# Performance work log

Measured on AMD Instinct MI355X. Metric: run time of the kernel, lower is better.

## Reference

```python
import jax, jax.numpy as jnp
import numpy as np

N_USERS = 50000
N_ITEMS = 100000
N_ENT = 200000
N_REL_TOTAL = 32  # n_relations * 2
DIM = 64
N_INTENTS = 2
N_LAYERS = 1
B = 4096
E_KG = 2_000_000
E_UI_HALF = 1_000_000  # user->item interactions; symmetrized to 2M directed edges


def setup_inputs() -> dict:
    key = jax.random.key(0)
    ks = jax.random.split(key, 16)
    s = 0.05  # xavier-ish scale
    user_emb = jax.random.normal(ks[0], (N_USERS, DIM), jnp.float32) * s
    entity_emb = jax.random.normal(ks[1], (N_ENT, DIM), jnp.float32) * s
    relation_emb = jax.random.normal(ks[2], (N_REL_TOTAL, DIM), jnp.float32) * s
    intent_weights = jax.random.normal(ks[3], (N_INTENTS, N_REL_TOTAL), jnp.float32) * s
    router_w = jax.random.normal(ks[4], (N_INTENTS, DIM), jnp.float32) * s
    router_b = jnp.zeros((N_INTENTS,), jnp.float32)
    kg_w = jax.random.normal(ks[5], (N_LAYERS, DIM, DIM), jnp.float32) * (1.0 / np.sqrt(DIM))
    item2entity = jax.random.randint(ks[6], (N_ITEMS,), 0, N_ENT)
    kg_src = jax.random.randint(ks[7], (E_KG,), 0, N_ENT)
    kg_dst = jax.random.randint(ks[8], (E_KG,), 0, N_ENT)
    kg_rel = jax.random.randint(ks[9], (E_KG,), 0, N_REL_TOTAL)
    # UI bipartite graph, symmetrically normalized (D^-1/2 A D^-1/2), as in _build_ui_graph
    rng = np.random.default_rng(0)
    uu = rng.integers(0, N_USERS, E_UI_HALF)
    ii = rng.integers(0, N_ITEMS, E_UI_HALF) + N_USERS
    rows = np.concatenate([uu, ii])
    cols = np.concatenate([ii, uu])
    n_nodes = N_USERS + N_ITEMS
    deg = np.bincount(rows, minlength=n_nodes).astype(np.float32)
    dinv = np.where(deg > 0, deg ** -0.5, 0.0).astype(np.float32)
    ui_vals = jnp.asarray(dinv[rows] * dinv[cols])
    ui_row = jnp.asarray(rows.astype(np.int32))
    ui_col = jnpseq = jnp.asarray(cols.astype(np.int32))
    u = jax.random.randint(ks[10], (B,), 0, N_USERS)
    i = jax.random.randint(ks[11], (B,), 0, N_ITEMS)
    neg_i = jax.random.randint(ks[12], (B,), 0, N_ITEMS)
    return dict(u=u, i=i, neg_i=neg_i,
                user_emb=user_emb, entity_emb=entity_emb, relation_emb=relation_emb,
                intent_weights=intent_weights, router_w=router_w, router_b=router_b,
                kg_w=kg_w, ui_vals=ui_vals,
                item2entity=item2entity, kg_src=kg_src, kg_dst=kg_dst, kg_rel=kg_rel,
                ui_row=ui_row, ui_col=ui_col)


def _l2norm(x):
    return x / jnp.maximum(jnp.linalg.norm(x, axis=-1, keepdims=True), 1e-12)


def reference(u, i, neg_i, user_emb, entity_emb, relation_emb, intent_weights,
              router_w, router_b, kg_w, ui_vals, item2entity, kg_src, kg_dst,
              kg_rel, ui_row, ui_col):
    n_ent = entity_emb.shape[0]
    # ---- _propagate_kg (dropout in eval mode = identity) ----
    x = entity_emb
    gate = jax.nn.sigmoid(relation_emb[kg_rel])  # [E, D]
    deg = jax.ops.segment_sum(jnp.ones(kg_dst.shape[0], jnp.float32), kg_dst,
                              num_segments=n_ent)
    deg = jnp.maximum(deg, 1.0)[:, None]
    for l in range(kg_w.shape[0]):
        msg = (x[kg_src] @ kg_w[l].T) * gate           # gather + linear + gate
        agg = jax.ops.segment_sum(msg, kg_dst, num_segments=n_ent)
        x = _l2norm(jax.nn.elu(agg / deg + x))
    item_kg = x[item2entity]                            # [n_items, D]
    # ---- _propagate_ui: sparse normalized adj propagation ----
    all_emb = jnp.concatenate([user_emb, item_kg], 0)
    n_nodes = all_emb.shape[0]
    embs = [all_emb]
    for _ in range(N_LAYERS):
        all_emb = jax.ops.segment_sum(ui_vals[:, None] * all_emb[ui_col], ui_row,
                                      num_segments=n_nodes)
        embs.append(all_emb)
    final = jnp.mean(jnp.stack(embs, 1), 1)
    n_users = user_emb.shape[0]
    u_prop, i_prop = final[:n_users], final[n_users:]
    # ---- intent mixing ----
    intent_dist = jax.nn.softmax(u_prop @ router_w.T + router_b, axis=-1)
    intent_emb = jax.nn.softmax(intent_weights, axis=-1) @ relation_emb
    ue = u_prop + intent_dist @ intent_emb
    ie = i_prop + item_kg
    pos = jnp.sum(ue[u] * ie[i], 1)
    neg = jnp.sum(ue[u] * ie[neg_i], 1)
    return pos, neg
```

## Files before the change

### kernel.cpp

```cpp
#include <hip/hip_runtime.h>
#include <math.h>

#define N_USERS 50000
#define N_ITEMS 100000
#define N_ENT   200000
#define N_NODES (N_USERS + N_ITEMS)
#define N_REL   32
#define DIM     64

#define NB_KG  391
#define NB_UI  586
#define NB_TOT (NB_KG + NB_UI)
#define CAPD   4096
#define NSCAT  768

__device__ __forceinline__ unsigned short f2bf(float f) {
    unsigned u = __float_as_uint(f);
    u += 0x7FFFu + ((u >> 16) & 1u);
    return (unsigned short)(u >> 16);
}
__device__ __forceinline__ float bf_lo(unsigned v) { return __uint_as_float(v << 16); }
__device__ __forceinline__ float bf_hi(unsigned v) { return __uint_as_float(v & 0xFFFF0000u); }
__device__ __forceinline__ int getbit(const unsigned* m, int i) {
    return (m[i >> 5] >> (i & 31)) & 1;
}

__global__ __launch_bounds__(512) void mm_scatter(const float* __restrict__ x,
                                                  const float* __restrict__ w,
                                                  unsigned short* __restrict__ y16,
                                                  int n_ent,
                                                  const int* __restrict__ kg_src,
                                                  const int* __restrict__ kg_dst,
                                                  const int* __restrict__ kg_rel,
                                                  const int* __restrict__ ui_row,
                                                  const int* __restrict__ ui_col,
                                                  const float* __restrict__ ui_vals,
                                                  const unsigned* __restrict__ ent_mask,
                                                  const unsigned* __restrict__ node_mask,
                                                  int* __restrict__ bcur,
                                                  unsigned int* __restrict__ kgrec,
                                                  int* __restrict__ uirec,
                                                  float* __restrict__ uval,
                                                  int e_kg, int e_ui) {
    __shared__ __align__(16) char smem[49152];
    int tid = threadIdx.x;

    if (blockIdx.x < NSCAT) {
        int* h     = (int*)smem;
        int* lbase = h + NB_TOT;
        int n = e_kg + e_ui;
        int nchunks = (n + 4095) >> 12;
        for (int c = blockIdx.x; c < nchunks; c += NSCAT) {
            int base = c << 12;
            for (int i = tid; i < NB_TOT; i += 512) h[i] = 0;
            __syncthreads();
            unsigned int rec[8];
            float val[8];
            int bk[8];
            #pragma unroll
            for (int j = 0; j < 8; j++) {
                int e = base + j * 512 + tid;
                bk[j] = -1;
                if (e < n) {
                    if (e < e_kg) {
                        int d = kg_dst[e];
                        if (getbit(ent_mask, d)) {
                            bk[j]  = d >> 9;
                            rec[j] = (unsigned int)kg_src[e]
                                     | ((unsigned int)kg_rel[e] << 18)
                                     | ((unsigned int)(d & 511) << 23);
                            atomicAdd(&h[bk[j]], 1);
                        }
                    } else {
                        int i2 = e - e_kg;
                        int r  = ui_row[i2];
                        if (getbit(node_mask, r)) {
                            bk[j]  = NB_KG + (r >> 8);
                            rec[j] = (unsigned int)ui_col[i2]
                                     | ((unsigned int)(r & 255) << 18);
                            val[j] = ui_vals[i2];
                            atomicAdd(&h[bk[j]], 1);
                        }
                    }
                }
            }
            __syncthreads();
            for (int i = tid; i < NB_TOT; i += 512) {
                int cc = h[i];
                lbase[i] = cc ? atomicAdd(&bcur[i], cc) : 0;
            }
            __syncthreads();
            #pragma unroll
            for (int j = 0; j < 8; j++) {
                if (bk[j] >= 0) {
                    int pos = atomicAdd(&lbase[bk[j]], 1);
                    if (bk[j] < NB_KG) kgrec[pos] = rec[j];
                    else               { uirec[pos] = (int)rec[j]; uval[pos] = val[j]; }
                }
            }
            __syncthreads();
        }
        return;
    }

    float (*xt)[128] = (float (*)[128])smem;
    float (*wt)[64]  = (float (*)[64])(smem + 32768);
    int base = (blockIdx.x - NSCAT) * 128;

    #pragma unroll
    for (int q = 0; q < 2; q++) {
        int idx = q * 512 + tid;
        int j = idx >> 4, k4 = idx & 15;
        int s0 = (k4 << 2) & 28;
        float4 v = ((const float4*)w)[idx];
        wt[4 * k4 + 0][j ^ s0] = v.x;
        wt[4 * k4 + 1][j ^ s0] = v.y;
        wt[4 * k4 + 2][j ^ s0] = v.z;
        wt[4 * k4 + 3][j ^ s0] = v.w;
    }
    #pragma unroll
    for (int q = 0; q < 4; q++) {
        int idx = q * 512 + tid;
        int r = idx >> 4, k4 = idx & 15;
        int gr = base + r;
        int s0 = (k4 << 2) & 28;
        if (gr < n_ent) {
            float4 v = ((const float4*)x)[(long)gr * 16 + k4];
            xt[4 * k4 + 0][r ^ s0] = v.x;
            xt[4 * k4 + 1][r ^ s0] = v.y;
            xt[4 * k4 + 2][r ^ s0] = v.z;
            xt[4 * k4 + 3][r ^ s0] = v.w;
        }
    }
    __syncthreads();

    int j0 = (tid & 7) * 8;
    int r0 = (tid >> 3) * 2;
    float acc[2][8];
    #pragma unroll
    for (int i = 0; i < 2; i++)
        #pragma unroll
        for (int j = 0; j < 8; j++) acc[i][j] = 0.f;

    #pragma unroll 4
    for (int k = 0; k < 64; k++) {
        int s = k & 28;
        float2 xa = *(const float2*)&xt[k][r0 ^ s];
        float4 wa = *(const float4*)&wt[k][j0 ^ s];
        float4 wb = *(const float4*)&wt[k][(j0 + 4) ^ s];
        float xr[2] = {xa.x, xa.y};
        float wr[8] = {wa.x, wa.y, wa.z, wa.w, wb.x, wb.y, wb.z, wb.w};
        #pragma unroll
        for (int i = 0; i < 2; i++)
            #pragma unroll
            for (int j = 0; j < 8; j++)
                acc[i][j] += xr[i] * wr[j];
    }

    #pragma unroll
    for (int i = 0; i < 2; i++) {
        int gr = base + r0 + i;
        if (gr < n_ent) {
            uint4 o;
            o.x = (unsigned)f2bf(acc[i][0]) | ((unsigned)f2bf(acc[i][1]) << 16);
            o.y = (unsigned)f2bf(acc[i][2]) | ((unsigned)f2bf(acc[i][3]) << 16);
            o.z = (unsigned)f2bf(acc[i][4]) | ((unsigned)f2bf(acc[i][5]) << 16);
            o.w = (unsigned)f2bf(acc[i][6]) | ((unsigned)f2bf(acc[i][7]) << 16);
            *(uint4*)&y16[(long)gr * 64 + j0] = o;
        }
    }
}

__global__ __launch_bounds__(256) void build_masks(const int* __restrict__ i2e,
                                                   const int* __restrict__ u,
                                                   const int* __restrict__ ipos,
                                                   const int* __restrict__ ineg,
                                                   unsigned* __restrict__ ent_mask,
                                                   unsigned* __restrict__ node_mask,
                                                   int* __restrict__ bcnt,
                                                   int B) {
    int t = blockIdx.x * 256 + threadIdx.x;
    int stride = gridDim.x * 256;
    for (int i = threadIdx.x; i < NB_TOT; i += 256) bcnt[i] = 0;
    for (int i = t; i < N_ITEMS; i += stride) {
        int e = i2e[i];
        atomicOr(&ent_mask[e >> 5], 1u << (e & 31));
    }
    for (int i = t; i < 3 * B; i += stride) {
        int r = (i < B) ? u[i]
              : (i < 2 * B) ? N_USERS + ipos[i - B]
                            : N_USERS + ineg[i - 2 * B];
        atomicOr(&node_mask[r >> 5], 1u << (r & 31));
    }
}

__global__ __launch_bounds__(256) void bucket_hist(const int* __restrict__ kg_dst,
                                                   const int* __restrict__ ui_row,
                                                   const unsigned* __restrict__ ent_mask,
                                                   const unsigned* __restrict__ node_mask,
                                                   const float* __restrict__ rel_emb,
                                                   float2* __restrict__ gateg,
                                                   int* __restrict__ bcnt,
                                                   int e_kg, int e_ui) {
    __shared__ int h[NB_TOT];
    for (int i = threadIdx.x; i < NB_TOT; i += 256) h[i] = 0;
    __syncthreads();
    if (blockIdx.x == 0) {
        for (int idx = threadIdx.x; idx < N_REL * 32; idx += 256) {
            int rel = idx >> 5, hl2 = idx & 31;
            float g0 = 1.0f / (1.0f + __expf(-rel_emb[rel * 64 + 2 * hl2]));
            float g1 = 1.0f / (1.0f + __expf(-rel_emb[rel * 64 + 2 * hl2 + 1]));
            gateg[idx] = make_float2(g0, g1);
        }
    }
    int n = e_kg + e_ui;
    int t = blockIdx.x * 256 + threadIdx.x;
    int stride = gridDim.x * 256;
    for (int e = t; e < n; e += stride) {
        int bk;
        if (e < e_kg) {
            int d = kg_dst[e];
            if (!getbit(ent_mask, d)) continue;
            bk = d >> 9;
        } else {
            int r = ui_row[e - e_kg];
            if (!getbit(node_mask, r)) continue;
            bk = NB_KG + (r >> 8);
        }
        atomicAdd(&h[bk], 1);
    }
    __syncthreads();
    for (int i = threadIdx.x; i < NB_TOT; i += 256)
        if (h[i]) atomicAdd(&bcnt[i], h[i]);
}

__global__ __launch_bounds__(256) void bucket_scan(const int* __restrict__ bcnt,
                                                   int* __restrict__ boff_kg,
                                                   int* __restrict__ boff_ui,
                                                   int* __restrict__ bcur) {
    __shared__ int sh[1024];
    int t = threadIdx.x;
    for (int seg = 0; seg < 2; seg++) {
        int NB = seg ? NB_UI : NB_KG;
        const int* src = bcnt + (seg ? NB_KG : 0);
        int idx[4] = { t, t + 256, t + 512, t + 768 };
        int v[4];
        #pragma unroll
        for (int q = 0; q < 4; q++) {
            v[q] = (idx[q] < NB) ? src[idx[q]] : 0;
            sh[idx[q]] = v[q];
        }
        __syncthreads();
        for (int o = 1; o < 1024; o <<= 1) {
            int a[4];
            #pragma unroll
            for (int q = 0; q < 4; q++) a[q] = (idx[q] >= o) ? sh[idx[q] - o] : 0;
            __syncthreads();
            #pragma unroll
            for (int q = 0; q < 4; q++) sh[idx[q]] += a[q];
            __syncthreads();
        }
        int* boff = seg ? boff_ui : boff_kg;
        int  base = seg ? NB_KG : 0;
        #pragma unroll
        for (int q = 0; q < 4; q++) {
            if (idx[q] < NB) {
                int ex = sh[idx[q]] - v[q];
                boff[idx[q]] = ex;
                bcur[base + idx[q]] = ex;
                if (idx[q] == NB - 1) boff[NB] = sh[idx[q]];
            }
        }
        __syncthreads();
    }
}

__global__ __launch_bounds__(256) void bucket_finalize(const int* __restrict__ boff_kg,
                                                       const int* __restrict__ boff_ui,
                                                       unsigned int* __restrict__ kgrec,
                                                       int* __restrict__ uirec,
                                                       float* __restrict__ uval,
                                                       int* __restrict__ off_kg,
                                                       int* __restrict__ off_ui) {
    __shared__ unsigned int rec[CAPD];
    __shared__ float fval[CAPD];
    __shared__ int hist[512];
    bool iskg = blockIdx.x < NB_KG;
    int  b    = iskg ? blockIdx.x : blockIdx.x - NB_KG;
    const int* boff = iskg ? boff_kg : boff_ui;
    int ebeg = boff[b], eend = boff[b + 1];
    int ne   = min(eend - ebeg, CAPD);
    int key_base = iskg ? (b << 9) : (b << 8);
    int nkeys = iskg ? min(512, N_ENT - key_base) : min(256, N_NODES - key_base);
    int SH = iskg ? 23 : 18;
    int tid = threadIdx.x;

    for (int i = tid; i < ne; i += 256) {
        if (iskg) rec[i] = kgrec[ebeg + i];
        else { rec[i] = (unsigned int)uirec[ebeg + i]; fval[i] = uval[ebeg + i]; }
    }
    for (int i = tid; i < 512; i += 256) hist[i] = 0;
    __syncthreads();
    for (int i = tid; i < ne; i += 256)
        atomicAdd(&hist[rec[i] >> SH], 1);
    __syncthreads();
    int i0 = tid, i1 = tid + 256;
    int v0 = hist[i0], v1 = hist[i1];
    __syncthreads();
    for (int o = 1; o < 512; o <<= 1) {
        int a0 = (i0 >= o) ? hist[i0 - o] : 0;
        int a1 = (i1 >= o) ? hist[i1 - o] : 0;
        __syncthreads();
        hist[i0] += a0; hist[i1] += a1;
        __syncthreads();
    }
    int e0 = hist[i0] - v0, e1 = hist[i1] - v1;
    __syncthreads();
    hist[i0] = e0; hist[i1] = e1;
    int* offg = iskg ? off_kg : off_ui;
    if (i0 < nkeys) offg[key_base + i0] = ebeg + e0;
    if (i1 < nkeys) offg[key_base + i1] = ebeg + e1;
    if (blockIdx.x == 0 && tid == 0) {
        off_kg[N_ENT]   = boff_kg[NB_KG];
        off_ui[N_NODES] = boff_ui[NB_UI];
    }
    __syncthreads();
    for (int i = tid; i < ne; i += 256) {
        unsigned int r = rec[i];
        int k = r >> SH;
        int slot = atomicAdd(&hist[k], 1);
        if (iskg) kgrec[ebeg + slot] = r & 0x7FFFFFu;
        else      { uirec[ebeg + slot] = (int)(r & 0x3FFFFu); uval[ebeg + slot] = fval[i]; }
    }
}

__global__ __launch_bounds__(256) void kgagg_build(const int* __restrict__ off,
                                                   const unsigned int* __restrict__ packed,
                                                   const unsigned short* __restrict__ y16,
                                                   const float* __restrict__ entity_emb,
                                                   const float* __restrict__ user_emb,
                                                   const int* __restrict__ i2e,
                                                   const float4* __restrict__ gate4,
                                                   const unsigned* __restrict__ node_mask,
                                                   float* __restrict__ all_emb,
                                                   unsigned short* __restrict__ all16) {
    int lane = threadIdx.x & 63;
    int half = lane >> 5;
    int hl   = lane & 31;
    int duo  = hl >> 4;
    int ql   = hl & 15;
    long wpair = (long)((blockIdx.x * 256 + threadIdx.x) >> 6);
    int w = (int)(wpair * 2 + half);
    if (w >= N_NODES) return;

    if (w < N_USERS) {
        if (duo == 0) {
            float4 v = ((const float4*)user_emb)[(long)w * 16 + ql];
            ((uint2*)all16)[(long)w * 16 + ql] =
                make_uint2((unsigned)f2bf(v.x) | ((unsigned)f2bf(v.y) << 16),
                           (unsigned)f2bf(v.z) | ((unsigned)f2bf(v.w) << 16));
        }
        return;
    }

    int ent = i2e[w - N_USERS];
    const uint2* y2 = (const uint2*)y16;
    int beg = off[ent], end = off[ent + 1];
    float a0 = 0.f, a1 = 0.f, a2 = 0.f, a3 = 0.f;
    float b0 = 0.f, b1 = 0.f, b2 = 0.f, b3 = 0.f;
    int p = beg;
    for (; p + 4 <= end; p += 4) {
        unsigned pk0 = packed[p + duo];
        unsigned pk1 = packed[p + 2 + duo];
        uint2 v0 = y2[(long)(pk0 & 0x3FFFF) * 16 + ql];
        uint2 v1 = y2[(long)(pk1 & 0x3FFFF) * 16 + ql];
        float4 g0 = gate4[(pk0 >> 18) * 16 + ql];
        float4 g1 = gate4[(pk1 >> 18) * 16 + ql];
        a0 += bf_lo(v0.x) * g0.x;  a1 += bf_hi(v0.x) * g0.y;
        a2 += bf_lo(v0.y) * g0.z;  a3 += bf_hi(v0.y) * g0.w;
        b0 += bf_lo(v1.x) * g1.x;  b1 += bf_hi(v1.x) * g1.y;
        b2 += bf_lo(v1.y) * g1.z;  b3 += bf_hi(v1.y) * g1.w;
    }
    if (p + duo < end) {
        unsigned pk = packed[p + duo];
        uint2 v = y2[(long)(pk & 0x3FFFF) * 16 + ql];
        float4 g = gate4[(pk >> 18) * 16 + ql];
        a0 += bf_lo(v.x) * g.x;  a1 += bf_hi(v.x) * g.y;
        a2 += bf_lo(v.y) * g.z;  a3 += bf_hi(v.y) * g.w;
    }
    if (p + 2 + duo < end) {
        unsigned pk = packed[p + 2 + duo];
        uint2 v = y2[(long)(pk & 0x3FFFF) * 16 + ql];
        float4 g = gate4[(pk >> 18) * 16 + ql];
        b0 += bf_lo(v.x) * g.x;  b1 += bf_hi(v.x) * g.y;
        b2 += bf_lo(v.y) * g.z;  b3 += bf_hi(v.y) * g.w;
    }
    a0 += b0; a1 += b1; a2 += b2; a3 += b3;
    a0 += __shfl_xor(a0, 16);
    a1 += __shfl_xor(a1, 16);
    a2 += __shfl_xor(a2, 16);
    a3 += __shfl_xor(a3, 16);

    float deg = fmaxf((float)(end - beg), 1.0f);
    float4 xv = ((const float4*)entity_emb)[(long)ent * 16 + ql];
    float v0 = a0 / deg + xv.x;
    float v1 = a1 / deg + xv.y;
    float v2 = a2 / deg + xv.z;
    float v3 = a3 / deg + xv.w;
    v0 = (v0 > 0.0f) ? v0 : (__expf(v0) - 1.0f);
    v1 = (v1 > 0.0f) ? v1 : (__expf(v1) - 1.0f);
    v2 = (v2 > 0.0f) ? v2 : (__expf(v2) - 1.0f);
    v3 = (v3 > 0.0f) ? v3 : (__expf(v3) - 1.0f);
    float ss = v0 * v0 + v1 * v1 + v2 * v2 + v3 * v3;
    ss += __shfl_xor(ss, 1);
    ss += __shfl_xor(ss, 2);
    ss += __shfl_xor(ss, 4);
    ss += __shfl_xor(ss, 8);
    float inv = 1.0f / fmaxf(sqrtf(ss), 1e-12f);
    if (duo == 0) {
        float r0 = v0 * inv, r1 = v1 * inv, r2 = v2 * inv, r3 = v3 * inv;
        if (getbit(node_mask, w))
            ((float4*)all_emb)[(long)w * 16 + ql] = make_float4(r0, r1, r2, r3);
        ((uint2*)all16)[(long)w * 16 + ql] =
            make_uint2((unsigned)f2bf(r0) | ((unsigned)f2bf(r1) << 16),
                       (unsigned)f2bf(r2) | ((unsigned)f2bf(r3) << 16));
    }
}

__global__ __launch_bounds__(256) void ui_aggregate_s(const int* __restrict__ off,
                                                      const int* __restrict__ colrec,
                                                      const float* __restrict__ uval,
                                                      const float* __restrict__ all_emb,
                                                      const float* __restrict__ user_emb,
                                                      const unsigned short* __restrict__ all16,
                                                      const int* __restrict__ u,
                                                      const int* __restrict__ ipos,
                                                      const int* __restrict__ ineg,
                                                      float* __restrict__ final_emb, int B) {
    const uint2* a2p = (const uint2*)all16;
    int lane = threadIdx.x & 63;
    int half = lane >> 5;
    int hl   = lane & 31;
    int duo  = hl >> 4;
    int ql   = hl & 15;
    long wpair = (long)((blockIdx.x * 256 + threadIdx.x) >> 6);
    int s = (int)(wpair * 2 + half);
    if (s >= 3 * B) return;
    int r;
    if (s < B)          r = u[s];
    else if (s < 2 * B) r = N_USERS + ipos[s - B];
    else                r = N_USERS + ineg[s - 2 * B];

    int beg = off[r], end = off[r + 1];
    float a0 = 0.f, a1 = 0.f, a2 = 0.f, a3 = 0.f;
    float b0 = 0.f, b1 = 0.f, b2 = 0.f, b3 = 0.f;
    int p = beg;
    for (; p + 4 <= end; p += 4) {
        int   c0 = colrec[p + duo];
        int   c1 = colrec[p + 2 + duo];
        float d0 = uval[p + duo];
        float d1 = uval[p + 2 + duo];
        uint2 v0 = a2p[(long)c0 * 16 + ql];
        uint2 v1 = a2p[(long)c1 * 16 + ql];
        a0 += d0 * bf_lo(v0.x);  a1 += d0 * bf_hi(v0.x);
        a2 += d0 * bf_lo(v0.y);  a3 += d0 * bf_hi(v0.y);
        b0 += d1 * bf_lo(v1.x);  b1 += d1 * bf_hi(v1.x);
        b2 += d1 * bf_lo(v1.y);  b3 += d1 * bf_hi(v1.y);
    }
    if (p + duo < end) {
        int   c = colrec[p + duo];
        float d = uval[p + duo];
        uint2 v = a2p[(long)c * 16 + ql];
        a0 += d * bf_lo(v.x);  a1 += d * bf_hi(v.x);
        a2 += d * bf_lo(v.y);  a3 += d * bf_hi(v.y);
    }
    if (p + 2 + duo < end) {
        int   c = colrec[p + 2 + duo];
        float d = uval[p + 2 + duo];
        uint2 v = a2p[(long)c * 16 + ql];
        b0 += d * bf_lo(v.x);  b1 += d * bf_hi(v.x);
        b2 += d * bf_lo(v.y);  b3 += d * bf_hi(v.y);
    }
    a0 += b0; a1 += b1; a2 += b2; a3 += b3;
    a0 += __shfl_xor(a0, 16);
    a1 += __shfl_xor(a1, 16);
    a2 += __shfl_xor(a2, 16);
    a3 += __shfl_xor(a3, 16);
    if (duo == 0) {
        float4 ae = (r < N_USERS)
            ? ((const float4*)user_emb)[(long)r * 16 + ql]
            : ((const float4*)all_emb)[(long)r * 16 + ql];
        ((float4*)final_emb)[(long)r * 16 + ql] =
            make_float4(0.5f * (ae.x + a0), 0.5f * (ae.y + a1),
                        0.5f * (ae.z + a2), 0.5f * (ae.w + a3));
    }
}

__global__ void final_kernel(const int* __restrict__ u, const int* __restrict__ ipos,
                             const int* __restrict__ ineg,
                             const float* __restrict__ final_emb,
                             const float* __restrict__ all_emb,
                             const float* __restrict__ rw, const float* __restrict__ rb,
                             const float* __restrict__ iw, const float* __restrict__ rel_emb,
                             float* __restrict__ out, int B) {
    __shared__ float sh_intent[128];
    if (threadIdx.x < 64) {
        int j = threadIdx.x;
        for (int k = 0; k < 2; k++) {
            float m = -1e30f;
            for (int r = 0; r < N_REL; r++) m = fmaxf(m, iw[k * N_REL + r]);
            float Z = 0.f, acc = 0.f;
            for (int r = 0; r < N_REL; r++) {
                float e = __expf(iw[k * N_REL + r] - m);
                Z += e;
                acc += e * rel_emb[r * 64 + j];
            }
            sh_intent[k * 64 + j] = acc / Z;
        }
    }
    __syncthreads();
    int lane = threadIdx.x & 63;
    int wave = (blockIdx.x * blockDim.x + threadIdx.x) >> 6;
    int nw   = (gridDim.x * blockDim.x) >> 6;
    for (int b = wave; b < B; b += nw) {
        int uu = u[b];
        float up = final_emb[(long)uu * 64 + lane];
        float l0 = up * rw[lane];
        float l1 = up * rw[64 + lane];
        #pragma unroll
        for (int o = 32; o; o >>= 1) {
            l0 += __shfl_xor(l0, o);
            l1 += __shfl_xor(l1, o);
        }
        l0 += rb[0]; l1 += rb[1];
        float m  = fmaxf(l0, l1);
        float e0 = __expf(l0 - m), e1 = __expf(l1 - m);
        float inv = 1.0f / (e0 + e1);
        float p0 = e0 * inv, p1 = e1 * inv;
        float ue = up + p0 * sh_intent[lane] + p1 * sh_intent[64 + lane];

        int it = ipos[b];
        long rr = (long)(N_USERS + it) * 64 + lane;
        float ie = final_emb[rr] + all_emb[rr];
        float dp = ue * ie;
        #pragma unroll
        for (int o = 32; o; o >>= 1) dp += __shfl_xor(dp, o);
        if (lane == 0) out[b] = dp;

        it = ineg[b];
        rr = (long)(N_USERS + it) * 64 + lane;
        ie = final_emb[rr] + all_emb[rr];
        dp = ue * ie;
        #pragma unroll
        for (int o = 32; o; o >>= 1) dp += __shfl_xor(dp, o);
        if (lane == 0) out[B + b] = dp;
    }
}

extern "C" void kernel_launch(void* const* d_in, const int* in_sizes, int n_in,
                              void* d_out, int out_size, void* d_ws, size_t ws_size,
                              hipStream_t stream) {
    const int*   u          = (const int*)  d_in[0];
    const int*   ipos       = (const int*)  d_in[1];
    const int*   ineg       = (const int*)  d_in[2];
    const float* user_emb   = (const float*)d_in[3];
    const float* entity_emb = (const float*)d_in[4];
    const float* rel_emb    = (const float*)d_in[5];
    const float* iw         = (const float*)d_in[6];
    const float* rw         = (const float*)d_in[7];
    const float* rb         = (const float*)d_in[8];
    const float* kgw        = (const float*)d_in[9];
    const float* ui_vals    = (const float*)d_in[10];
    const int*   i2e        = (const int*)  d_in[11];
    const int*   kg_src     = (const int*)  d_in[12];
    const int*   kg_dst     = (const int*)  d_in[13];
    const int*   kg_rel     = (const int*)  d_in[14];
    const int*   ui_row     = (const int*)  d_in[15];
    const int*   ui_col     = (const int*)  d_in[16];
    float*       out        = (float*)d_out;

    int B    = in_sizes[0];
    int e_kg = in_sizes[12];
    int e_ui = in_sizes[15];

    char* ws = (char*)d_ws;
    unsigned short* y16       = (unsigned short*)(ws + 0);
    float*          all_emb   = (float*)(ws + 25600000);
    unsigned short* all16     = (unsigned short*)(ws + 64000000);
    float*          final_emb = (float*)(ws + 83200000);
    unsigned int*   kgrec     = (unsigned int*)(ws + 121600000);
    int*            uirec     = (int*)(ws + 129600000);
    float*          uval      = (float*)(ws + 133600000);
    int*            off_kg    = (int*)(ws + 137600000);
    int*            off_ui    = (int*)(ws + 138400256);
    unsigned*       ent_mask  = (unsigned*)(ws + 139000512);
    unsigned*       node_mask = (unsigned*)(ws + 139025600);
    int*            bcnt      = (int*)(ws + 139600512);
    int*            boff_kg   = (int*)(ws + 139604480);
    int*            boff_ui   = (int*)(ws + 139606272);
    int*            bcur      = (int*)(ws + 139608704);
    float2*         gateg     = (float2*)(ws + 139612672);

    hipMemsetAsync(ent_mask, 0, 25088 + 18752, stream);
    build_masks    <<<512, 256, 0, stream>>>(i2e, u, ipos, ineg, ent_mask, node_mask,
                                             bcnt, B);
    bucket_hist    <<<1024, 256, 0, stream>>>(kg_dst, ui_row, ent_mask, node_mask,
                                              rel_emb, gateg, bcnt, e_kg, e_ui);
    bucket_scan    <<<1,   256, 0, stream>>>(bcnt, boff_kg, boff_ui, bcur);
    mm_scatter     <<<NSCAT + (N_ENT + 127) / 128, 512, 0, stream>>>(
        entity_emb, kgw, y16, N_ENT,
        kg_src, kg_dst, kg_rel, ui_row, ui_col, ui_vals,
        ent_mask, node_mask, bcur, kgrec, uirec, uval, e_kg, e_ui);
    bucket_finalize<<<NB_TOT, 256, 0, stream>>>(boff_kg, boff_ui, kgrec, uirec, uval,
                                                off_kg, off_ui);

    {
        int nwaves = (N_NODES + 1) / 2;
        int nblk   = (nwaves * 64 + 255) / 256;
        kgagg_build<<<nblk, 256, 0, stream>>>(
            off_kg, kgrec, y16, entity_emb, user_emb, i2e, (const float4*)gateg,
            node_mask, all_emb, all16);
    }
    {
        int nwaves = (3 * B + 1) / 2;
        int nblk   = (nwaves * 64 + 255) / 256;
        ui_aggregate_s<<<nblk, 256, 0, stream>>>(
            off_ui, uirec, uval, all_emb, user_emb, all16, u, ipos, ineg, final_emb, B);
    }
    final_kernel<<<256, 256, 0, stream>>>(u, ipos, ineg, final_emb, all_emb,
                                          rw, rb, iw, rel_emb, out, B);
}
```

Measured before the change: 313.8 us.

## Replace bucket histogram and scan with fixed-capacity buckets and interleaved scatter/matmul blocks

Drops the bucket_hist and bucket_scan kernels by giving each destination bucket a fixed capacity slot (CAPK for KG, CAPU for UI), so the scatter can start from precomputed bucket bases. Per-row begin/end arrays replace the prefix offsets. Scatter blocks are also interleaved one in three with matmul tile blocks so both kinds of work run together on the GPU. This saves a full pass over the 4M edge indices and two kernel launches, but any edges beyond a bucket's capacity are silently dropped, which risks wrong results if a bucket overflows.

New measurement: 279.8 us. -10.8%, faster.

```diff
diff --git a/kernel.cpp b/kernel.cpp
--- a/kernel.cpp
+++ b/kernel.cpp
@@ -11,8 +11,11 @@
 #define NB_KG  391
 #define NB_UI  586
 #define NB_TOT (NB_KG + NB_UI)
-#define CAPD   4096
-#define NSCAT  768
+#define CAPK   4096
+#define CAPU   1536
+#define NMMTILE 1563
+#define NSCAT3  782
+#define FUSE_GRID (NSCAT3 * 3)
 
 __device__ __forceinline__ unsigned short f2bf(float f) {
     unsigned u = __float_as_uint(f);
@@ -23,6 +26,40 @@
 __device__ __forceinline__ float bf_hi(unsigned v) { return __uint_as_float(v & 0xFFFF0000u); }
 __device__ __forceinline__ int getbit(const unsigned* m, int i) {
     return (m[i >> 5] >> (i & 31)) & 1;
+}
+
+__global__ __launch_bounds__(256) void build_masks(const int* __restrict__ i2e,
+                                                   const int* __restrict__ u,
+                                                   const int* __restrict__ ipos,
+                                                   const int* __restrict__ ineg,
+                                                   const float* __restrict__ rel_emb,
+                                                   float2* __restrict__ gateg,
+                                                   unsigned* __restrict__ ent_mask,
+                                                   unsigned* __restrict__ node_mask,
+                                                   int* __restrict__ bcur,
+                                                   int B) {
+    int t = blockIdx.x * 256 + threadIdx.x;
+    int stride = gridDim.x * 256;
+    for (int i = threadIdx.x; i < NB_TOT; i += 256)
+        bcur[i] = (i < NB_KG) ? i * CAPK : (i - NB_KG) * CAPU;
+    if (blockIdx.x == 0) {
+        for (int idx = threadIdx.x; idx < N_REL * 32; idx += 256) {
+            int rel = idx >> 5, hl2 = idx & 31;
+            float g0 = 1.0f / (1.0f + __expf(-rel_emb[rel * 64 + 2 * hl2]));
+            float g1 = 1.0f / (1.0f + __expf(-rel_emb[rel * 64 + 2 * hl2 + 1]));
+            gateg[idx] = make_float2(g0, g1);
+        }
+    }
+    for (int i = t; i < N_ITEMS; i += stride) {
+        int e = i2e[i];
+        atomicOr(&ent_mask[e >> 5], 1u << (e & 31));
+    }
+    for (int i = t; i < 3 * B; i += stride) {
+        int r = (i < B) ? u[i]
+              : (i < 2 * B) ? N_USERS + ipos[i - B]
+                            : N_USERS + ineg[i - 2 * B];
+        atomicOr(&node_mask[r >> 5], 1u << (r & 31));
+    }
 }
 
 __global__ __launch_bounds__(512) void mm_scatter(const float* __restrict__ x,
@@ -44,13 +81,14 @@
                                                   int e_kg, int e_ui) {
     __shared__ __align__(16) char smem[49152];
     int tid = threadIdx.x;
-
-    if (blockIdx.x < NSCAT) {
+    int bid = blockIdx.x;
+
+    if (bid % 3 == 0) {
         int* h     = (int*)smem;
         int* lbase = h + NB_TOT;
         int n = e_kg + e_ui;
         int nchunks = (n + 4095) >> 12;
-        for (int c = blockIdx.x; c < nchunks; c += NSCAT) {
+        for (int c = bid / 3; c < nchunks; c += NSCAT3) {
             int base = c << 12;
             for (int i = tid; i < NB_TOT; i += 512) h[i] = 0;
             __syncthreads();
@@ -94,8 +132,12 @@
             for (int j = 0; j < 8; j++) {
                 if (bk[j] >= 0) {
                     int pos = atomicAdd(&lbase[bk[j]], 1);
-                    if (bk[j] < NB_KG) kgrec[pos] = rec[j];
-                    else               { uirec[pos] = (int)rec[j]; uval[pos] = val[j]; }
+                    if (bk[j] < NB_KG) {
+                        if (pos < (bk[j] + 1) * CAPK) kgrec[pos] = rec[j];
+                    } else {
+                        int bu = bk[j] - NB_KG;
+                        if (pos < (bu + 1) * CAPU) { uirec[pos] = (int)rec[j]; uval[pos] = val[j]; }
+                    }
                 }
             }
             __syncthreads();
@@ -103,9 +145,11 @@
         return;
     }
 
+    int mtile = bid - bid / 3 - 1;
+    if (mtile >= NMMTILE) return;
     float (*xt)[128] = (float (*)[128])smem;
     float (*wt)[64]  = (float (*)[64])(smem + 32768);
-    int base = (blockIdx.x - NSCAT) * 128;
+    int base = mtile * 128;
 
     #pragma unroll
     for (int q = 0; q < 2; q++) {
@@ -171,133 +215,30 @@
     }
 }
 
-__global__ __launch_bounds__(256) void build_masks(const int* __restrict__ i2e,
-                                                   const int* __restrict__ u,
-                                                   const int* __restrict__ ipos,
-                                                   const int* __restrict__ ineg,
-                                                   unsigned* __restrict__ ent_mask,
-                                                   unsigned* __restrict__ node_mask,
-                                                   int* __restrict__ bcnt,
-                                                   int B) {
-    int t = blockIdx.x * 256 + threadIdx.x;
-    int stride = gridDim.x * 256;
-    for (int i = threadIdx.x; i < NB_TOT; i += 256) bcnt[i] = 0;
-    for (int i = t; i < N_ITEMS; i += stride) {
-        int e = i2e[i];
-        atomicOr(&ent_mask[e >> 5], 1u << (e & 31));
-    }
-    for (int i = t; i < 3 * B; i += stride) {
-        int r = (i < B) ? u[i]
-              : (i < 2 * B) ? N_USERS + ipos[i - B]
-                            : N_USERS + ineg[i - 2 * B];
-        atomicOr(&node_mask[r >> 5], 1u << (r & 31));
-    }
-}
-
-__global__ __launch_bounds__(256) void bucket_hist(const int* __restrict__ kg_dst,
-                                                   const int* __restrict__ ui_row,
-                                                   const unsigned* __restrict__ ent_mask,
-                                                   const unsigned* __restrict__ node_mask,
-                                                   const float* __restrict__ rel_emb,
-                                                   float2* __restrict__ gateg,
-                                                   int* __restrict__ bcnt,
-                                                   int e_kg, int e_ui) {
-    __shared__ int h[NB_TOT];
-    for (int i = threadIdx.x; i < NB_TOT; i += 256) h[i] = 0;
-    __syncthreads();
-    if (blockIdx.x == 0) {
-        for (int idx = threadIdx.x; idx < N_REL * 32; idx += 256) {
-            int rel = idx >> 5, hl2 = idx & 31;
-            float g0 = 1.0f / (1.0f + __expf(-rel_emb[rel * 64 + 2 * hl2]));
-            float g1 = 1.0f / (1.0f + __expf(-rel_emb[rel * 64 + 2 * hl2 + 1]));
-            gateg[idx] = make_float2(g0, g1);
-        }
-    }
-    int n = e_kg + e_ui;
-    int t = blockIdx.x * 256 + threadIdx.x;
-    int stride = gridDim.x * 256;
-    for (int e = t; e < n; e += stride) {
-        int bk;
-        if (e < e_kg) {
-            int d = kg_dst[e];
-            if (!getbit(ent_mask, d)) continue;
-            bk = d >> 9;
-        } else {
-            int r = ui_row[e - e_kg];
-            if (!getbit(node_mask, r)) continue;
-            bk = NB_KG + (r >> 8);
-        }
-        atomicAdd(&h[bk], 1);
-    }
-    __syncthreads();
-    for (int i = threadIdx.x; i < NB_TOT; i += 256)
-        if (h[i]) atomicAdd(&bcnt[i], h[i]);
-}
-
-__global__ __launch_bounds__(256) void bucket_scan(const int* __restrict__ bcnt,
-                                                   int* __restrict__ boff_kg,
-                                                   int* __restrict__ boff_ui,
-                                                   int* __restrict__ bcur) {
-    __shared__ int sh[1024];
-    int t = threadIdx.x;
-    for (int seg = 0; seg < 2; seg++) {
-        int NB = seg ? NB_UI : NB_KG;
-        const int* src = bcnt + (seg ? NB_KG : 0);
-        int idx[4] = { t, t + 256, t + 512, t + 768 };
-        int v[4];
-        #pragma unroll
-        for (int q = 0; q < 4; q++) {
-            v[q] = (idx[q] < NB) ? src[idx[q]] : 0;
-            sh[idx[q]] = v[q];
-        }
-        __syncthreads();
-        for (int o = 1; o < 1024; o <<= 1) {
-            int a[4];
-            #pragma unroll
-            for (int q = 0; q < 4; q++) a[q] = (idx[q] >= o) ? sh[idx[q] - o] : 0;
-            __syncthreads();
-            #pragma unroll
-            for (int q = 0; q < 4; q++) sh[idx[q]] += a[q];
-            __syncthreads();
-        }
-        int* boff = seg ? boff_ui : boff_kg;
-        int  base = seg ? NB_KG : 0;
-        #pragma unroll
-        for (int q = 0; q < 4; q++) {
-            if (idx[q] < NB) {
-                int ex = sh[idx[q]] - v[q];
-                boff[idx[q]] = ex;
-                bcur[base + idx[q]] = ex;
-                if (idx[q] == NB - 1) boff[NB] = sh[idx[q]];
-            }
-        }
-        __syncthreads();
-    }
-}
-
-__global__ __launch_bounds__(256) void bucket_finalize(const int* __restrict__ boff_kg,
-                                                       const int* __restrict__ boff_ui,
+__global__ __launch_bounds__(256) void bucket_finalize(const int* __restrict__ bcur,
                                                        unsigned int* __restrict__ kgrec,
                                                        int* __restrict__ uirec,
                                                        float* __restrict__ uval,
-                                                       int* __restrict__ off_kg,
-                                                       int* __restrict__ off_ui) {
-    __shared__ unsigned int rec[CAPD];
-    __shared__ float fval[CAPD];
+                                                       int* __restrict__ beg_kg,
+                                                       int* __restrict__ end_kg,
+                                                       int* __restrict__ beg_ui,
+                                                       int* __restrict__ end_ui) {
+    __shared__ unsigned int rec[CAPK];
+    __shared__ float fval[CAPU];
     __shared__ int hist[512];
     bool iskg = blockIdx.x < NB_KG;
     int  b    = iskg ? blockIdx.x : blockIdx.x - NB_KG;
-    const int* boff = iskg ? boff_kg : boff_ui;
-    int ebeg = boff[b], eend = boff[b + 1];
-    int ne   = min(eend - ebeg, CAPD);
+    int base  = iskg ? b * CAPK : b * CAPU;
+    int cap   = iskg ? CAPK : CAPU;
+    int ne    = min(bcur[blockIdx.x] - base, cap);
     int key_base = iskg ? (b << 9) : (b << 8);
     int nkeys = iskg ? min(512, N_ENT - key_base) : min(256, N_NODES - key_base);
     int SH = iskg ? 23 : 18;
     int tid = threadIdx.x;
 
     for (int i = tid; i < ne; i += 256) {
-        if (iskg) rec[i] = kgrec[ebeg + i];
-        else { rec[i] = (unsigned int)uirec[ebeg + i]; fval[i] = uval[ebeg + i]; }
+        if (iskg) rec[i] = kgrec[base + i];
+        else { rec[i] = (unsigned int)uirec[base + i]; fval[i] = uval[base + i]; }
     }
     for (int i = tid; i < 512; i += 256) hist[i] = 0;
     __syncthreads();
@@ -317,24 +258,22 @@
     int e0 = hist[i0] - v0, e1 = hist[i1] - v1;
     __syncthreads();
     hist[i0] = e0; hist[i1] = e1;
-    int* offg = iskg ? off_kg : off_ui;
-    if (i0 < nkeys) offg[key_base + i0] = ebeg + e0;
-    if (i1 < nkeys) offg[key_base + i1] = ebeg + e1;
-    if (blockIdx.x == 0 && tid == 0) {
-        off_kg[N_ENT]   = boff_kg[NB_KG];
-        off_ui[N_NODES] = boff_ui[NB_UI];
-    }
+    int* begg = iskg ? beg_kg : beg_ui;
+    int* endg = iskg ? end_kg : end_ui;
+    if (i0 < nkeys) { begg[key_base + i0] = base + e0; endg[key_base + i0] = base + e0 + v0; }
+    if (i1 < nkeys) { begg[key_base + i1] = base + e1; endg[key_base + i1] = base + e1 + v1; }
     __syncthreads();
     for (int i = tid; i < ne; i += 256) {
         unsigned int r = rec[i];
         int k = r >> SH;
         int slot = atomicAdd(&hist[k], 1);
-        if (iskg) kgrec[ebeg + slot] = r & 0x7FFFFFu;
-        else      { uirec[ebeg + slot] = (int)(r & 0x3FFFFu); uval[ebeg + slot] = fval[i]; }
-    }
-}
-
-__global__ __launch_bounds__(256) void kgagg_build(const int* __restrict__ off,
+        if (iskg) kgrec[base + slot] = r & 0x7FFFFFu;
+        else      { uirec[base + slot] = (int)(r & 0x3FFFFu); uval[base + slot] = fval[i]; }
+    }
+}
+
+__global__ __launch_bounds__(256) void kgagg_build(const int* __restrict__ beg_kg,
+                                                   const int* __restrict__ end_kg,
                                                    const unsigned int* __restrict__ packed,
                                                    const unsigned short* __restrict__ y16,
                                                    const float* __restrict__ entity_emb,
@@ -365,7 +304,7 @@
 
     int ent = i2e[w - N_USERS];
     const uint2* y2 = (const uint2*)y16;
-    int beg = off[ent], end = off[ent + 1];
+    int beg = beg_kg[ent], end = end_kg[ent];
     float a0 = 0.f, a1 = 0.f, a2 = 0.f, a3 = 0.f;
     float b0 = 0.f, b1 = 0.f, b2 = 0.f, b3 = 0.f;
     int p = beg;
@@ -427,7 +366,8 @@
     }
 }
 
-__global__ __launch_bounds__(256) void ui_aggregate_s(const int* __restrict__ off,
+__global__ __launch_bounds__(256) void ui_aggregate_s(const int* __restrict__ beg_ui,
+                                                      const int* __restrict__ end_ui,
                                                       const int* __restrict__ colrec,
                                                       const float* __restrict__ uval,
                                                       const float* __restrict__ all_emb,
@@ -451,7 +391,7 @@
     else if (s < 2 * B) r = N_USERS + ipos[s - B];
     else                r = N_USERS + ineg[s - 2 * B];
 
-    int beg = off[r], end = off[r + 1];
+    int beg = beg_ui[r], end = end_ui[r];
     float a0 = 0.f, a1 = 0.f, a2 = 0.f, a3 = 0.f;
     float b0 = 0.f, b1 = 0.f, b2 = 0.f, b3 = 0.f;
     int p = beg;
@@ -589,43 +529,39 @@
     unsigned short* all16     = (unsigned short*)(ws + 64000000);
     float*          final_emb = (float*)(ws + 83200000);
     unsigned int*   kgrec     = (unsigned int*)(ws + 121600000);
+    int*            end_kg    = (int*)(ws + 128006144);
+    int*            end_ui    = (int*)(ws + 128806144);
     int*            uirec     = (int*)(ws + 129600000);
     float*          uval      = (float*)(ws + 133600000);
-    int*            off_kg    = (int*)(ws + 137600000);
-    int*            off_ui    = (int*)(ws + 138400256);
+    int*            beg_kg    = (int*)(ws + 137600000);
+    int*            beg_ui    = (int*)(ws + 138400256);
     unsigned*       ent_mask  = (unsigned*)(ws + 139000512);
     unsigned*       node_mask = (unsigned*)(ws + 139025600);
-    int*            bcnt      = (int*)(ws + 139600512);
-    int*            boff_kg   = (int*)(ws + 139604480);
-    int*            boff_ui   = (int*)(ws + 139606272);
     int*            bcur      = (int*)(ws + 139608704);
     float2*         gateg     = (float2*)(ws + 139612672);
 
     hipMemsetAsync(ent_mask, 0, 25088 + 18752, stream);
-    build_masks    <<<512, 256, 0, stream>>>(i2e, u, ipos, ineg, ent_mask, node_mask,
-                                             bcnt, B);
-    bucket_hist    <<<1024, 256, 0, stream>>>(kg_dst, ui_row, ent_mask, node_mask,
-                                              rel_emb, gateg, bcnt, e_kg, e_ui);
-    bucket_scan    <<<1,   256, 0, stream>>>(bcnt, boff_kg, boff_ui, bcur);
-    mm_scatter     <<<NSCAT + (N_ENT + 127) / 128, 512, 0, stream>>>(
+    build_masks<<<512, 256, 0, stream>>>(i2e, u, ipos, ineg, rel_emb, gateg,
+                                         ent_mask, node_mask, bcur, B);
+    mm_scatter <<<FUSE_GRID, 512, 0, stream>>>(
         entity_emb, kgw, y16, N_ENT,
         kg_src, kg_dst, kg_rel, ui_row, ui_col, ui_vals,
         ent_mask, node_mask, bcur, kgrec, uirec, uval, e_kg, e_ui);
-    bucket_finalize<<<NB_TOT, 256, 0, stream>>>(boff_kg, boff_ui, kgrec, uirec, uval,
-                                                off_kg, off_ui);
-
+    bucket_finalize<<<NB_TOT, 256, 0, stream>>>(bcur, kgrec, uirec, uval,
+                                                beg_kg, end_kg, beg_ui, end_ui);
     {
         int nwaves = (N_NODES + 1) / 2;
         int nblk   = (nwaves * 64 + 255) / 256;
         kgagg_build<<<nblk, 256, 0, stream>>>(
-            off_kg, kgrec, y16, entity_emb, user_emb, i2e, (const float4*)gateg,
-            node_mask, all_emb, all16);
+            beg_kg, end_kg, kgrec, y16, entity_emb, user_emb, i2e,
+            (const float4*)gateg, node_mask, all_emb, all16);
     }
     {
         int nwaves = (3 * B + 1) / 2;
         int nblk   = (nwaves * 64 + 255) / 256;
         ui_aggregate_s<<<nblk, 256, 0, stream>>>(
-            off_ui, uirec, uval, all_emb, user_emb, all16, u, ipos, ineg, final_emb, B);
+            beg_ui, end_ui, uirec, uval, all_emb, user_emb, all16,
+            u, ipos, ineg, final_emb, B);
     }
     final_kernel<<<256, 256, 0, stream>>>(u, ipos, ineg, final_emb, all_emb,
                                           rw, rb, iw, rel_emb, out, B);
```
